# Optimization experiments

Measured on AMD Instinct MI355X. Metric: run time of the kernel, lower is better.

The kernel has to match this reference:

```python
import jax, jax.numpy as jnp
import numpy as np

B, N, E, H, D, F = 2, 4096, 128, 8, 16, 512
EPS = 1e-6


def _rms_norm(x, w):
    xf = x.astype(jnp.float32)
    n = xf * jax.lax.rsqrt(jnp.mean(xf * xf, axis=-1, keepdims=True) + EPS)
    return n.astype(x.dtype) * w


def setup_inputs() -> dict:
    key = jax.random.key(0)
    ks = jax.random.split(key, 12)
    s = 1.0 / np.sqrt(E)
    sf = 1.0 / np.sqrt(F)
    coords = jax.random.uniform(ks[10], (B, N, 2))
    dis = jnp.sqrt(jnp.sum((coords[:, :, None, :] - coords[:, None, :, :]) ** 2, -1))
    dis = dis * (1.0 - jnp.eye(N))  # zero diagonal
    return {
        "input1": jax.random.normal(ks[0], (B, N, E), jnp.float32),
        "dis_matrix": dis.astype(jnp.float32),
        "Wq": jax.random.uniform(ks[1], (E, E), jnp.float32, -s, s),
        "Wk": jax.random.uniform(ks[2], (E, E), jnp.float32, -s, s),
        "Wv": jax.random.uniform(ks[3], (E, E), jnp.float32, -s, s),
        "alpha": jnp.float32(1.0),
        "ln1_w": jnp.ones((E,), jnp.float32),
        "ln2_w": jnp.ones((E,), jnp.float32),
        "Wcomb": jax.random.uniform(ks[4], (E, E), jnp.float32, -s, s),
        "W1": jax.random.uniform(ks[5], (F, E), jnp.float32, -s, s),
        "b1": jax.random.uniform(ks[6], (F,), jnp.float32, -s, s),
        "W2": jax.random.uniform(ks[7], (E, F), jnp.float32, -sf, sf),
        "b2": jax.random.uniform(ks[8], (E,), jnp.float32, -sf, sf),
    }


def _sparse_attention_afm(x, dis_matrix, Wq, Wk, Wv, alpha):
    # project and split heads: [B,N,E] -> [B,H,N,D]
    def heads(w):
        return (x @ w.T).reshape(B, N, H, D).transpose(0, 2, 1, 3)
    q, k, v = heads(Wq), heads(Wk), heads(Wv)
    log2n = jnp.float32(np.log2(N))
    dis_weight = jnp.exp(-alpha * log2n * dis_matrix)  # [B,N,N] (i,j)
    k_weight = jnp.exp(k)  # [B,H,N,D]
    w1 = jnp.einsum('bij,bhik->bhjk', dis_weight, k_weight * v)
    w2 = jnp.einsum('bij,bhik->bhjk', dis_weight, k_weight)
    out = jax.nn.sigmoid(q) * (w1 / w2)  # [B,H,N,D]
    return out.transpose(0, 2, 1, 3).reshape(B, N, E)


def reference(input1, dis_matrix, Wq, Wk, Wv, alpha, ln1_w, ln2_w, Wcomb, W1, b1, W2, b2):
    h = _rms_norm(input1, ln1_w)
    attn = _sparse_attention_afm(h, dis_matrix, Wq, Wk, Wv, alpha)
    out1 = input1 + attn @ Wcomb.T
    h2 = _rms_norm(out1, ln2_w)
    ffn = jax.nn.relu(h2 @ W1.T + b1) @ W2.T + b2
    return out1 + ffn
```

## Files before the change

kernel.cpp:

```cpp
#include <hip/hip_runtime.h>

#define NTOK 4096
#define EDIM 128

typedef __attribute__((ext_vector_type(8))) short bf16x8;
typedef __attribute__((ext_vector_type(4))) float f32x4;

__device__ __forceinline__ ushort f2bf(float x) {
    union { float f; unsigned u; } c; c.f = x;
    unsigned r = c.u + 0x7FFF + ((c.u >> 16) & 1);
    return (ushort)(r >> 16);
}

__device__ __forceinline__ int swz64(int r, int k)  { return r * 64  + (k ^ ((r & 7) << 3)); }
__device__ __forceinline__ int swz128(int r, int k) { return r * 128 + (k ^ ((r & 7) << 3)); }

__device__ __forceinline__ void stage_w(const float* __restrict__ W, ushort* Bs) {
    const int t = threadIdx.x;
    const int br = t >> 1, h = (t & 1) * 64;
    const float* src = W + (size_t)br * 128 + h;
    ushort* dst = Bs + br * 136 + h;
#pragma unroll
    for (int j = 0; j < 8; ++j) {
        float4 u = *(const float4*)(src + j * 8);
        float4 v = *(const float4*)(src + j * 8 + 4);
        bf16x8 o;
        o[0] = (short)f2bf(u.x); o[1] = (short)f2bf(u.y);
        o[2] = (short)f2bf(u.z); o[3] = (short)f2bf(u.w);
        o[4] = (short)f2bf(v.x); o[5] = (short)f2bf(v.y);
        o[6] = (short)f2bf(v.z); o[7] = (short)f2bf(v.w);
        *(bf16x8*)(dst + j * 8) = o;
    }
}

__device__ __forceinline__ void gemm128(const ushort* __restrict__ As,
                                        const ushort* __restrict__ Bs,
                                        f32x4 (&acc)[2][2], int lane, int wv) {
    const int m15 = lane & 15, kq = (lane >> 4) * 8, c0w = wv * 32;
#pragma unroll
    for (int kc = 0; kc < 4; ++kc) {
        int ko = kc * 32 + kq;
        bf16x8 a0 = *(const bf16x8*)&As[m15 * 136 + ko];
        bf16x8 a1 = *(const bf16x8*)&As[(16 + m15) * 136 + ko];
        bf16x8 b0 = *(const bf16x8*)&Bs[(c0w + m15) * 136 + ko];
        bf16x8 b1 = *(const bf16x8*)&Bs[(c0w + 16 + m15) * 136 + ko];
        acc[0][0] = __builtin_amdgcn_mfma_f32_16x16x32_bf16(a0, b0, acc[0][0], 0, 0, 0);
        acc[0][1] = __builtin_amdgcn_mfma_f32_16x16x32_bf16(a0, b1, acc[0][1], 0, 0, 0);
        acc[1][0] = __builtin_amdgcn_mfma_f32_16x16x32_bf16(a1, b0, acc[1][0], 0, 0, 0);
        acc[1][1] = __builtin_amdgcn_mfma_f32_16x16x32_bf16(a1, b1, acc[1][1], 0, 0, 0);
    }
}

__device__ __forceinline__ void gemm_dirB(const ushort* __restrict__ As,
                                          const ushort* __restrict__ W, int ldb,
                                          f32x4 (&acc)[2][2], int lane, int wv) {
    const int m15 = lane & 15, kq = (lane >> 4) * 8, c0w = wv * 32;
#pragma unroll
    for (int kc = 0; kc < 4; ++kc) {
        int ko = kc * 32 + kq;
        bf16x8 a0 = *(const bf16x8*)&As[swz128(m15, ko)];
        bf16x8 a1 = *(const bf16x8*)&As[swz128(16 + m15, ko)];
        bf16x8 b0 = *(const bf16x8*)&W[(size_t)(c0w + m15) * ldb + ko];
        bf16x8 b1 = *(const bf16x8*)&W[(size_t)(c0w + 16 + m15) * ldb + ko];
        acc[0][0] = __builtin_amdgcn_mfma_f32_16x16x32_bf16(a0, b0, acc[0][0], 0, 0, 0);
        acc[0][1] = __builtin_amdgcn_mfma_f32_16x16x32_bf16(a0, b1, acc[0][1], 0, 0, 0);
        acc[1][0] = __builtin_amdgcn_mfma_f32_16x16x32_bf16(a1, b0, acc[1][0], 0, 0, 0);
        acc[1][1] = __builtin_amdgcn_mfma_f32_16x16x32_bf16(a1, b1, acc[1][1], 0, 0, 0);
    }
}

__launch_bounds__(256, 2)
__global__ void qkv_k(const float* __restrict__ input1, const float* __restrict__ ln1w,
                      const float* __restrict__ Wq, const float* __restrict__ Wk,
                      const float* __restrict__ Wv,
                      const float* __restrict__ Wc, const float* __restrict__ W1,
                      const float* __restrict__ W2, ushort* __restrict__ Wbf,
                      float* __restrict__ sigq, ushort* __restrict__ Mt) {
    const int bx = blockIdx.x;
    if (bx >= 256) {
        int g = ((bx - 256) * 256 + threadIdx.x) * 4;
        const float* src; ushort* dst;
        if (g < 16384)      { src = Wc + g;           dst = Wbf + 49152 + g; }
        else if (g < 81920) { src = W1 + (g - 16384); dst = Wbf + 65536 + (g - 16384); }
        else                { src = W2 + (g - 81920); dst = Wbf + 131072 + (g - 81920); }
        float4 u = *(const float4*)src;
        ushort4 o; o.x = f2bf(u.x); o.y = f2bf(u.y); o.z = f2bf(u.z); o.w = f2bf(u.w);
        *(ushort4*)dst = o;
        return;
    }
    __shared__ ushort As[32 * 136];
    __shared__ ushort Bs0[128 * 136];
    __shared__ ushort Bs1[128 * 136];
    const int t = threadIdx.x, lane = t & 63, wv = t >> 6;
    const int m15 = lane & 15, quad = lane >> 4, c0w = wv * 32;
    const int M0 = bx * 32;

    {
        const int row = t >> 3, seg = t & 7;
        const float* xp = input1 + (size_t)(M0 + row) * 128 + seg * 16;
        float4 x[4]; float ss = 0.f;
#pragma unroll
        for (int i = 0; i < 4; ++i) {
            x[i] = *(const float4*)(xp + i * 4);
            ss += x[i].x * x[i].x + x[i].y * x[i].y + x[i].z * x[i].z + x[i].w * x[i].w;
        }
        ss += __shfl_down(ss, 4, 8);
        ss += __shfl_down(ss, 2, 8);
        ss += __shfl_down(ss, 1, 8);
        ss = __shfl(ss, 0, 8);
        float rr = rsqrtf(ss * (1.0f / 128.0f) + 1e-6f);
#pragma unroll
        for (int i = 0; i < 4; ++i) {
            float4 w4 = *(const float4*)&ln1w[seg * 16 + i * 4];
            ushort4 o;
            o.x = f2bf(x[i].x * rr * w4.x);
            o.y = f2bf(x[i].y * rr * w4.y);
            o.z = f2bf(x[i].z * rr * w4.z);
            o.w = f2bf(x[i].w * rr * w4.w);
            *(ushort4*)&As[row * 136 + seg * 16 + i * 4] = o;
        }
    }
    stage_w(Wq, Bs0);
    __syncthreads();
    {
        f32x4 acc[2][2] = {};
        gemm128(As, Bs0, acc, lane, wv);
        stage_w(Wk, Bs1);
#pragma unroll
        for (int mi = 0; mi < 2; ++mi)
#pragma unroll
            for (int ni = 0; ni < 2; ++ni)
#pragma unroll
                for (int r = 0; r < 4; ++r) {
                    int row = M0 + mi * 16 + quad * 4 + r;
                    int lc  = c0w + ni * 16 + m15;
                    sigq[(size_t)row * 128 + lc] = 1.0f / (1.0f + __expf(-acc[mi][ni][r]));
                }
    }
    __syncthreads();
    f32x4 acck[2][2] = {};
    gemm128(As, Bs1, acck, lane, wv);
    stage_w(Wv, Bs0);
    __syncthreads();
    f32x4 accv[2][2] = {};
    gemm128(As, Bs0, accv, lane, wv);
    const int b = M0 >> 12, i0 = M0 & (NTOK - 1);
#pragma unroll
    for (int mi = 0; mi < 2; ++mi)
#pragma unroll
        for (int ni = 0; ni < 2; ++ni) {
            int e = c0w + ni * 16 + m15;
            ushort* mt0 = Mt + ((size_t)b * 256 + e) * NTOK;
            ushort* mt1 = mt0 + (size_t)128 * NTOK;
            int ib = i0 + mi * 16 + quad * 4;
            ushort4 pv, pk;
            float kw0 = __expf(acck[mi][ni][0]); pv.x = f2bf(kw0 * accv[mi][ni][0]); pk.x = f2bf(kw0);
            float kw1 = __expf(acck[mi][ni][1]); pv.y = f2bf(kw1 * accv[mi][ni][1]); pk.y = f2bf(kw1);
            float kw2 = __expf(acck[mi][ni][2]); pv.z = f2bf(kw2 * accv[mi][ni][2]); pk.z = f2bf(kw2);
            float kw3 = __expf(acck[mi][ni][3]); pv.w = f2bf(kw3 * accv[mi][ni][3]); pk.w = f2bf(kw3);
            *(ushort4*)&mt0[ib] = pv;
            *(ushort4*)&mt1[ib] = pk;
        }
}

__launch_bounds__(512, 2)
__global__ void big_gemm_k(const float* __restrict__ dis, const float* __restrict__ alphap,
                           const ushort* __restrict__ Mt,
                           float* __restrict__ P0, float* __restrict__ P1) {
    __shared__ ushort As[2][64 * 64];
    const int t = threadIdx.x, lane = t & 63, wv = t >> 6;
    const int m15 = lane & 15, quad = lane >> 4, kq = quad * 8;
    const int b  = blockIdx.x & 1;
    const int s  = (blockIdx.x >> 1) & 1;
    const int j0 = (blockIdx.x >> 2) * 64;
    const float coefl2 = -alphap[0] * 12.0f * 1.44269504088896f;
    const float* disb = dis + (size_t)b * NTOK * NTOK;
    const ushort* Mtb = Mt + (size_t)b * 256 * NTOK;
    float* outp = ((s == 0) ? P0 : P1) + (size_t)b * NTOK * 256;
    const int k0 = s * (NTOK / 2);

    const int sr = t >> 3, sk = (t & 7) * 8;
    const float* arow = disb + (size_t)(j0 + sr) * NTOK + k0 + sk;
    const int c0 = wv * 32;
    const ushort* Bp = Mtb + (size_t)(c0 + m15) * NTOK + k0 + kq;
    const ushort* Bp1 = Bp + (size_t)16 * NTOK;

    f32x4 acc[4][2] = {};
    float4 fa0, fa1, fb0, fb1;
    bf16x8 pb[2][2], pbn[2][2];

    {
        float4 g0 = *(const float4*)(arow);
        float4 g1 = *(const float4*)(arow + 4);
        bf16x8 a8;
        a8[0] = (short)f2bf(exp2f(coefl2 * g0.x));
        a8[1] = (short)f2bf(exp2f(coefl2 * g0.y));
        a8[2] = (short)f2bf(exp2f(coefl2 * g0.z));
        a8[3] = (short)f2bf(exp2f(coefl2 * g0.w));
        a8[4] = (short)f2bf(exp2f(coefl2 * g1.x));
        a8[5] = (short)f2bf(exp2f(coefl2 * g1.y));
        a8[6] = (short)f2bf(exp2f(coefl2 * g1.z));
        a8[7] = (short)f2bf(exp2f(coefl2 * g1.w));
        *(bf16x8*)&As[0][swz64(sr, sk)] = a8;
        fa0 = *(const float4*)(arow + 64);
        fa1 = *(const float4*)(arow + 68);
#pragma unroll
        for (int kh = 0; kh < 2; ++kh) {
            pb[kh][0] = *(const bf16x8*)&Bp[kh * 32];
            pb[kh][1] = *(const bf16x8*)&Bp1[kh * 32];
        }
        __syncthreads();
    }

#define BIG_ITER(FAc0, FAc1, FAn0, FAn1, PBC, PBN, BUFC, BUFN, IT) do {         \
    {   int ia = (IT) + 2; int ka = (ia < 32) ? ia * 64 : 0;                    \
        FAn0 = *(const float4*)(arow + ka);                                     \
        FAn1 = *(const float4*)(arow + ka + 4);                                 \
        int ib = (IT) + 1; int kb_ = (ib < 32) ? ib * 64 : 0;                   \
        _Pragma("unroll") for (int kh = 0; kh < 2; ++kh) {                      \
            PBN[kh][0] = *(const bf16x8*)&Bp[kb_ + kh * 32];                    \
            PBN[kh][1] = *(const bf16x8*)&Bp1[kb_ + kh * 32];                   \
        } }                                                                     \
    __builtin_amdgcn_sched_barrier(0);                                          \
    {   bf16x8 a8;                                                              \
        a8[0] = (short)f2bf(exp2f(coefl2 * FAc0.x));                            \
        a8[1] = (short)f2bf(exp2f(coefl2 * FAc0.y));                            \
        a8[2] = (short)f2bf(exp2f(coefl2 * FAc0.z));                            \
        a8[3] = (short)f2bf(exp2f(coefl2 * FAc0.w));                            \
        a8[4] = (short)f2bf(exp2f(coefl2 * FAc1.x));                            \
        a8[5] = (short)f2bf(exp2f(coefl2 * FAc1.y));                            \
        a8[6] = (short)f2bf(exp2f(coefl2 * FAc1.z));                            \
        a8[7] = (short)f2bf(exp2f(coefl2 * FAc1.w));                            \
        *(bf16x8*)&BUFN[swz64(sr, sk)] = a8; }                                  \
    _Pragma("unroll") for (int kh = 0; kh < 2; ++kh) {                          \
        bf16x8 a0 = *(const bf16x8*)&BUFC[swz64(m15,      kh * 32 + kq)];       \
        bf16x8 a1 = *(const bf16x8*)&BUFC[swz64(16 + m15, kh * 32 + kq)];       \
        bf16x8 a2 = *(const bf16x8*)&BUFC[swz64(32 + m15, kh * 32 + kq)];       \
        bf16x8 a3 = *(const bf16x8*)&BUFC[swz64(48 + m15, kh * 32 + kq)];       \
        acc[0][0] = __builtin_amdgcn_mfma_f32_16x16x32_bf16(a0, PBC[kh][0], acc[0][0], 0, 0, 0); \
        acc[0][1] = __builtin_amdgcn_mfma_f32_16x16x32_bf16(a0, PBC[kh][1], acc[0][1], 0, 0, 0); \
        acc[1][0] = __builtin_amdgcn_mfma_f32_16x16x32_bf16(a1, PBC[kh][0], acc[1][0], 0, 0, 0); \
        acc[1][1] = __builtin_amdgcn_mfma_f32_16x16x32_bf16(a1, PBC[kh][1], acc[1][1], 0, 0, 0); \
        acc[2][0] = __builtin_amdgcn_mfma_f32_16x16x32_bf16(a2, PBC[kh][0], acc[2][0], 0, 0, 0); \
        acc[2][1] = __builtin_amdgcn_mfma_f32_16x16x32_bf16(a2, PBC[kh][1], acc[2][1], 0, 0, 0); \
        acc[3][0] = __builtin_amdgcn_mfma_f32_16x16x32_bf16(a3, PBC[kh][0], acc[3][0], 0, 0, 0); \
        acc[3][1] = __builtin_amdgcn_mfma_f32_16x16x32_bf16(a3, PBC[kh][1], acc[3][1], 0, 0, 0); \
    }                                                                           \
    __builtin_amdgcn_sched_barrier(0);                                          \
    asm volatile("s_waitcnt lgkmcnt(0)" ::: "memory");                          \
    __builtin_amdgcn_s_barrier();                                               \
    __builtin_amdgcn_sched_barrier(0);                                          \
} while (0)

#pragma unroll 1
    for (int u = 0; u < 16; ++u) {
        int IT = u * 2;
        BIG_ITER(fa0, fa1, fb0, fb1, pb, pbn, As[0], As[1], IT);
        BIG_ITER(fb0, fb1, fa0, fa1, pbn, pb, As[1], As[0], IT + 1);
    }
#undef BIG_ITER

#pragma unroll
    for (int mi = 0; mi < 4; ++mi)
#pragma unroll
        for (int ni = 0; ni < 2; ++ni)
#pragma unroll
            for (int r = 0; r < 4; ++r) {
                int j = j0 + mi * 16 + quad * 4 + r;
                int c = c0 + ni * 16 + m15;
                outp[(size_t)j * 256 + c] = acc[mi][ni][r];
            }
}

__launch_bounds__(256, 1)
__global__ void tail_k(const float* __restrict__ sigq,
                       const float* __restrict__ P0, const float* __restrict__ P1,
                       const ushort* __restrict__ Wbf,
                       const float* __restrict__ input1, const float* __restrict__ b1,
                       const float* __restrict__ b2, const float* __restrict__ ln2w,
                       float* __restrict__ out) {
    __shared__ ushort As[32 * 128];
    __shared__ ushort As2[32 * 128];
    __shared__ float  O[32][132];
    const int t = threadIdx.x, lane = t & 63, wv = t >> 6;
    const int m15 = lane & 15, quad = lane >> 4, c0w = wv * 32;
    const int M0 = blockIdx.x * 32;

    {
        const int ar = t >> 3, e0 = (t & 7) * 16;
        const int g = M0 + ar;
        const float4* sg  = (const float4*)(sigq + (size_t)g * 128 + e0);
        const float4* p0a = (const float4*)(P0 + (size_t)g * 256 + e0);
        const float4* p1a = (const float4*)(P1 + (size_t)g * 256 + e0);
        const float4* p0b = (const float4*)(P0 + (size_t)g * 256 + 128 + e0);
        const float4* p1b = (const float4*)(P1 + (size_t)g * 256 + 128 + e0);
#pragma unroll
        for (int i = 0; i < 4; ++i) {
            float4 s = sg[i];
            float4 u0 = p0a[i], u1 = p1a[i], d0 = p0b[i], d1 = p1b[i];
            ushort4 a;
            a.x = f2bf(s.x * (u0.x + u1.x) / (d0.x + d1.x));
            a.y = f2bf(s.y * (u0.y + u1.y) / (d0.y + d1.y));
            a.z = f2bf(s.z * (u0.z + u1.z) / (d0.z + d1.z));
            a.w = f2bf(s.w * (u0.w + u1.w) / (d0.w + d1.w));
            *(ushort4*)&As[swz128(ar, e0 + i * 4)] = a;
        }
    }
    __syncthreads();
    f32x4 acc[2][2] = {};
    gemm_dirB(As, Wbf + 49152, 128, acc, lane, wv);
#pragma unroll
    for (int mi = 0; mi < 2; ++mi)
#pragma unroll
        for (int ni = 0; ni < 2; ++ni)
#pragma unroll
            for (int r = 0; r < 4; ++r) {
                int rl  = mi * 16 + quad * 4 + r;
                int col = c0w + ni * 16 + m15;
                O[rl][col] = acc[mi][ni][r] + input1[(size_t)(M0 + rl) * 128 + col];
            }
    __syncthreads();
    {
        const int row = t >> 3, seg = t & 7;
        float4 x[4]; float ss = 0.f;
#pragma unroll
        for (int i = 0; i < 4; ++i) {
            x[i] = *(const float4*)&O[row][seg * 16 + i * 4];
            ss += x[i].x * x[i].x + x[i].y * x[i].y + x[i].z * x[i].z + x[i].w * x[i].w;
        }
        ss += __shfl_down(ss, 4, 8);
        ss += __shfl_down(ss, 2, 8);
        ss += __shfl_down(ss, 1, 8);
        ss = __shfl(ss, 0, 8);
        float rr = rsqrtf(ss * (1.0f / 128.0f) + 1e-6f);
#pragma unroll
        for (int i = 0; i < 4; ++i) {
            float4 w4 = *(const float4*)&ln2w[seg * 16 + i * 4];
            ushort4 o;
            o.x = f2bf(x[i].x * rr * w4.x);
            o.y = f2bf(x[i].y * rr * w4.y);
            o.z = f2bf(x[i].z * rr * w4.z);
            o.w = f2bf(x[i].w * rr * w4.w);
            *(ushort4*)&As[swz128(row, seg * 16 + i * 4)] = o;
        }
    }
    f32x4 aout[2][2] = {};
    for (int f0 = 0; f0 < 4; ++f0) {
        __syncthreads();
        f32x4 am[2][2] = {};
        gemm_dirB(As, Wbf + 65536 + f0 * 128 * 128, 128, am, lane, wv);
#pragma unroll
        for (int mi = 0; mi < 2; ++mi)
#pragma unroll
            for (int ni = 0; ni < 2; ++ni)
#pragma unroll
                for (int r = 0; r < 4; ++r) {
                    int rl  = mi * 16 + quad * 4 + r;
                    int col = c0w + ni * 16 + m15;
                    As2[swz128(rl, col)] = f2bf(fmaxf(am[mi][ni][r] + b1[f0 * 128 + col], 0.0f));
                }
        __syncthreads();
        gemm_dirB(As2, Wbf + 131072 + f0 * 128, 512, aout, lane, wv);
    }
#pragma unroll
    for (int mi = 0; mi < 2; ++mi)
#pragma unroll
        for (int ni = 0; ni < 2; ++ni)
#pragma unroll
            for (int r = 0; r < 4; ++r) {
                int rl  = mi * 16 + quad * 4 + r;
                int col = c0w + ni * 16 + m15;
                out[(size_t)(M0 + rl) * 128 + col] = (O[rl][col] + b2[col]) + aout[mi][ni][r];
            }
}

extern "C" void kernel_launch(void* const* d_in, const int* in_sizes, int n_in,
                              void* d_out, int out_size, void* d_ws, size_t ws_size,
                              hipStream_t stream) {
    const float* input1 = (const float*)d_in[0];
    const float* dis    = (const float*)d_in[1];
    const float* Wq     = (const float*)d_in[2];
    const float* Wk     = (const float*)d_in[3];
    const float* Wv     = (const float*)d_in[4];
    const float* alpha  = (const float*)d_in[5];
    const float* ln1    = (const float*)d_in[6];
    const float* ln2    = (const float*)d_in[7];
    const float* Wcomb  = (const float*)d_in[8];
    const float* W1     = (const float*)d_in[9];
    const float* b1     = (const float*)d_in[10];
    const float* W2     = (const float*)d_in[11];
    const float* b2     = (const float*)d_in[12];
    float* out = (float*)d_out;

    char* w8 = (char*)d_ws;
    ushort* Wbf  = (ushort*)(w8);
    float*  sigq = (float*)(w8 + (4u << 20));
    ushort* Mt   = (ushort*)(w8 + (8u << 20));
    float*  P0   = (float*)(w8 + (12u << 20));
    float*  P1   = (float*)(w8 + (20u << 20));

    qkv_k<<<dim3(400), 256, 0, stream>>>(input1, ln1, Wq, Wk, Wv,
                                         Wcomb, W1, W2, Wbf, sigq, Mt);
    big_gemm_k<<<dim3(256), 512, 0, stream>>>(dis, alpha, Mt, P0, P1);
    tail_k<<<dim3(256), 256, 0, stream>>>(sigq, P0, P1, Wbf, input1, b1, b2,
                                          ln2, out);
}
```

Measured before the change: 258.3 us.

## Split big GEMM K dimension four ways and halve tail tile rows

The main dis-weighted GEMM now splits its K reduction into four slices instead of two, launching 512 blocks that write four partial buffers. The tail kernel sums all four partials and processes 16 rows per block instead of 32, also launching 512 blocks. Both changes aim to fill more of the GPU's compute units. The cost is extra partial-sum traffic (two more 8MB buffers written and read), smaller MFMA tiles in the tail with less weight reuse, and higher occupancy hints that may constrain registers.

```diff
diff --git a/kernel.cpp b/kernel.cpp
--- a/kernel.cpp
+++ b/kernel.cpp
@@ -51,21 +51,18 @@
     }
 }
 
-__device__ __forceinline__ void gemm_dirB(const ushort* __restrict__ As,
-                                          const ushort* __restrict__ W, int ldb,
-                                          f32x4 (&acc)[2][2], int lane, int wv) {
+__device__ __forceinline__ void gemm16_dirB(const ushort* __restrict__ As,
+                                            const ushort* __restrict__ W, int ldb,
+                                            f32x4 (&acc)[2], int lane, int wv) {
     const int m15 = lane & 15, kq = (lane >> 4) * 8, c0w = wv * 32;
 #pragma unroll
     for (int kc = 0; kc < 4; ++kc) {
         int ko = kc * 32 + kq;
         bf16x8 a0 = *(const bf16x8*)&As[swz128(m15, ko)];
-        bf16x8 a1 = *(const bf16x8*)&As[swz128(16 + m15, ko)];
         bf16x8 b0 = *(const bf16x8*)&W[(size_t)(c0w + m15) * ldb + ko];
         bf16x8 b1 = *(const bf16x8*)&W[(size_t)(c0w + 16 + m15) * ldb + ko];
-        acc[0][0] = __builtin_amdgcn_mfma_f32_16x16x32_bf16(a0, b0, acc[0][0], 0, 0, 0);
-        acc[0][1] = __builtin_amdgcn_mfma_f32_16x16x32_bf16(a0, b1, acc[0][1], 0, 0, 0);
-        acc[1][0] = __builtin_amdgcn_mfma_f32_16x16x32_bf16(a1, b0, acc[1][0], 0, 0, 0);
-        acc[1][1] = __builtin_amdgcn_mfma_f32_16x16x32_bf16(a1, b1, acc[1][1], 0, 0, 0);
+        acc[0] = __builtin_amdgcn_mfma_f32_16x16x32_bf16(a0, b0, acc[0], 0, 0, 0);
+        acc[1] = __builtin_amdgcn_mfma_f32_16x16x32_bf16(a0, b1, acc[1], 0, 0, 0);
     }
 }
 
@@ -163,26 +160,27 @@
         }
 }
 
-__launch_bounds__(512, 2)
+__launch_bounds__(512, 4)
 __global__ void big_gemm_k(const float* __restrict__ dis, const float* __restrict__ alphap,
                            const ushort* __restrict__ Mt,
-                           float* __restrict__ P0, float* __restrict__ P1) {
+                           float* __restrict__ P0, float* __restrict__ P1,
+                           float* __restrict__ P2, float* __restrict__ P3) {
     __shared__ ushort As[2][64 * 64];
     const int t = threadIdx.x, lane = t & 63, wv = t >> 6;
     const int m15 = lane & 15, quad = lane >> 4, kq = quad * 8;
     const int b  = blockIdx.x & 1;
-    const int s  = (blockIdx.x >> 1) & 1;
-    const int j0 = (blockIdx.x >> 2) * 64;
+    const int s  = (blockIdx.x >> 1) & 3;
+    const int j0 = (blockIdx.x >> 3) * 64;
     const float coefl2 = -alphap[0] * 12.0f * 1.44269504088896f;
     const float* disb = dis + (size_t)b * NTOK * NTOK;
     const ushort* Mtb = Mt + (size_t)b * 256 * NTOK;
-    float* outp = ((s == 0) ? P0 : P1) + (size_t)b * NTOK * 256;
-    const int k0 = s * (NTOK / 2);
+    float* outp = (s == 0 ? P0 : s == 1 ? P1 : s == 2 ? P2 : P3) + (size_t)b * NTOK * 256;
+    const int k0 = s * (NTOK / 4);
 
     const int sr = t >> 3, sk = (t & 7) * 8;
     const float* arow = disb + (size_t)(j0 + sr) * NTOK + k0 + sk;
     const int c0 = wv * 32;
-    const ushort* Bp = Mtb + (size_t)(c0 + m15) * NTOK + k0 + kq;
+    const ushort* Bp  = Mtb + (size_t)(c0 + m15) * NTOK + k0 + kq;
     const ushort* Bp1 = Bp + (size_t)16 * NTOK;
 
     f32x4 acc[4][2] = {};
@@ -213,10 +211,10 @@
     }
 
 #define BIG_ITER(FAc0, FAc1, FAn0, FAn1, PBC, PBN, BUFC, BUFN, IT) do {         \
-    {   int ia = (IT) + 2; int ka = (ia < 32) ? ia * 64 : 0;                    \
+    {   int ia = (IT) + 2; int ka = (ia < 16) ? ia * 64 : 0;                    \
         FAn0 = *(const float4*)(arow + ka);                                     \
         FAn1 = *(const float4*)(arow + ka + 4);                                 \
-        int ib = (IT) + 1; int kb_ = (ib < 32) ? ib * 64 : 0;                   \
+        int ib = (IT) + 1; int kb_ = (ib < 16) ? ib * 64 : 0;                   \
         _Pragma("unroll") for (int kh = 0; kh < 2; ++kh) {                      \
             PBN[kh][0] = *(const bf16x8*)&Bp[kb_ + kh * 32];                    \
             PBN[kh][1] = *(const bf16x8*)&Bp1[kb_ + kh * 32];                   \
@@ -253,7 +251,7 @@
 } while (0)
 
 #pragma unroll 1
-    for (int u = 0; u < 16; ++u) {
+    for (int u = 0; u < 8; ++u) {
         int IT = u * 2;
         BIG_ITER(fa0, fa1, fb0, fb1, pb, pbn, As[0], As[1], IT);
         BIG_ITER(fb0, fb1, fa0, fa1, pbn, pb, As[1], As[0], IT + 1);
@@ -272,106 +270,109 @@
             }
 }
 
-__launch_bounds__(256, 1)
+__launch_bounds__(256, 2)
 __global__ void tail_k(const float* __restrict__ sigq,
                        const float* __restrict__ P0, const float* __restrict__ P1,
+                       const float* __restrict__ P2, const float* __restrict__ P3,
                        const ushort* __restrict__ Wbf,
                        const float* __restrict__ input1, const float* __restrict__ b1,
                        const float* __restrict__ b2, const float* __restrict__ ln2w,
                        float* __restrict__ out) {
-    __shared__ ushort As[32 * 128];
-    __shared__ ushort As2[32 * 128];
-    __shared__ float  O[32][132];
+    __shared__ ushort As[16 * 128];
+    __shared__ ushort As2[16 * 128];
+    __shared__ float  O[16][132];
     const int t = threadIdx.x, lane = t & 63, wv = t >> 6;
     const int m15 = lane & 15, quad = lane >> 4, c0w = wv * 32;
-    const int M0 = blockIdx.x * 32;
+    const int M0 = blockIdx.x * 16;
 
     {
-        const int ar = t >> 3, e0 = (t & 7) * 16;
+        const int ar = t >> 4, e0 = (t & 15) * 8;
         const int g = M0 + ar;
-        const float4* sg  = (const float4*)(sigq + (size_t)g * 128 + e0);
-        const float4* p0a = (const float4*)(P0 + (size_t)g * 256 + e0);
-        const float4* p1a = (const float4*)(P1 + (size_t)g * 256 + e0);
-        const float4* p0b = (const float4*)(P0 + (size_t)g * 256 + 128 + e0);
-        const float4* p1b = (const float4*)(P1 + (size_t)g * 256 + 128 + e0);
-#pragma unroll
-        for (int i = 0; i < 4; ++i) {
-            float4 s = sg[i];
-            float4 u0 = p0a[i], u1 = p1a[i], d0 = p0b[i], d1 = p1b[i];
+        const float* sg = sigq + (size_t)g * 128 + e0;
+        const float* pu0 = P0 + (size_t)g * 256 + e0;
+        const float* pu1 = P1 + (size_t)g * 256 + e0;
+        const float* pu2 = P2 + (size_t)g * 256 + e0;
+        const float* pu3 = P3 + (size_t)g * 256 + e0;
+#pragma unroll
+        for (int i = 0; i < 2; ++i) {
+            float4 s  = *(const float4*)(sg + i * 4);
+            float4 u0 = *(const float4*)(pu0 + i * 4);
+            float4 u1 = *(const float4*)(pu1 + i * 4);
+            float4 u2 = *(const float4*)(pu2 + i * 4);
+            float4 u3 = *(const float4*)(pu3 + i * 4);
+            float4 d0 = *(const float4*)(pu0 + 128 + i * 4);
+            float4 d1 = *(const float4*)(pu1 + 128 + i * 4);
+            float4 d2 = *(const float4*)(pu2 + 128 + i * 4);
+            float4 d3 = *(const float4*)(pu3 + 128 + i * 4);
             ushort4 a;
-            a.x = f2bf(s.x * (u0.x + u1.x) / (d0.x + d1.x));
-            a.y = f2bf(s.y * (u0.y + u1.y) / (d0.y + d1.y));
-            a.z = f2bf(s.z * (u0.z + u1.z) / (d0.z + d1.z));
-            a.w = f2bf(s.w * (u0.w + u1.w) / (d0.w + d1.w));
+            a.x = f2bf(s.x * ((u0.x + u1.x) + (u2.x + u3.x)) / ((d0.x + d1.x) + (d2.x + d3.x)));
+            a.y = f2bf(s.y * ((u0.y + u1.y) + (u2.y + u3.y)) / ((d0.y + d1.y) + (d2.y + d3.y)));
+            a.z = f2bf(s.z * ((u0.z + u1.z) + (u2.z + u3.z)) / ((d0.z + d1.z) + (d2.z + d3.z)));
+            a.w = f2bf(s.w * ((u0.w + u1.w) + (u2.w + u3.w)) / ((d0.w + d1.w) + (d2.w + d3.w)));
             *(ushort4*)&As[swz128(ar, e0 + i * 4)] = a;
         }
     }
     __syncthreads();
-    f32x4 acc[2][2] = {};
-    gemm_dirB(As, Wbf + 49152, 128, acc, lane, wv);
-#pragma unroll
-    for (int mi = 0; mi < 2; ++mi)
-#pragma unroll
-        for (int ni = 0; ni < 2; ++ni)
-#pragma unroll
-            for (int r = 0; r < 4; ++r) {
-                int rl  = mi * 16 + quad * 4 + r;
-                int col = c0w + ni * 16 + m15;
-                O[rl][col] = acc[mi][ni][r] + input1[(size_t)(M0 + rl) * 128 + col];
-            }
+    f32x4 acc[2] = {};
+    gemm16_dirB(As, Wbf + 49152, 128, acc, lane, wv);
+#pragma unroll
+    for (int ni = 0; ni < 2; ++ni)
+#pragma unroll
+        for (int r = 0; r < 4; ++r) {
+            int rl  = quad * 4 + r;
+            int col = c0w + ni * 16 + m15;
+            O[rl][col] = acc[ni][r] + input1[(size_t)(M0 + rl) * 128 + col];
+        }
     __syncthreads();
     {
-        const int row = t >> 3, seg = t & 7;
-        float4 x[4]; float ss = 0.f;
-#pragma unroll
-        for (int i = 0; i < 4; ++i) {
-            x[i] = *(const float4*)&O[row][seg * 16 + i * 4];
+        const int row = t >> 4, seg = t & 15;
+        float4 x[2]; float ss = 0.f;
+#pragma unroll
+        for (int i = 0; i < 2; ++i) {
+            x[i] = *(const float4*)&O[row][seg * 8 + i * 4];
             ss += x[i].x * x[i].x + x[i].y * x[i].y + x[i].z * x[i].z + x[i].w * x[i].w;
         }
-        ss += __shfl_down(ss, 4, 8);
-        ss += __shfl_down(ss, 2, 8);
-        ss += __shfl_down(ss, 1, 8);
-        ss = __shfl(ss, 0, 8);
+        ss += __shfl_down(ss, 8, 16);
+        ss += __shfl_down(ss, 4, 16);
+        ss += __shfl_down(ss, 2, 16);
+        ss += __shfl_down(ss, 1, 16);
+        ss = __shfl(ss, 0, 16);
         float rr = rsqrtf(ss * (1.0f / 128.0f) + 1e-6f);
 #pragma unroll
-        for (int i = 0; i < 4; ++i) {
-            float4 w4 = *(const float4*)&ln2w[seg * 16 + i * 4];
+        for (int i = 0; i < 2; ++i) {
+            float4 w4 = *(const float4*)&ln2w[seg * 8 + i * 4];
             ushort4 o;
             o.x = f2bf(x[i].x * rr * w4.x);
             o.y = f2bf(x[i].y * rr * w4.y);
             o.z = f2bf(x[i].z * rr * w4.z);
             o.w = f2bf(x[i].w * rr * w4.w);
-            *(ushort4*)&As[swz128(row, seg * 16 + i * 4)] = o;
-        }
-    }
-    f32x4 aout[2][2] = {};
+            *(ushort4*)&As[swz128(row, seg * 8 + i * 4)] = o;
+        }
+    }
+    f32x4 aout[2] = {};
     for (int f0 = 0; f0 < 4; ++f0) {
         __syncthreads();
-        f32x4 am[2][2] = {};
-        gemm_dirB(As, Wbf + 65536 + f0 * 128 * 128, 128, am, lane, wv);
-#pragma unroll
-        for (int mi = 0; mi < 2; ++mi)
-#pragma unroll
-            for (int ni = 0; ni < 2; ++ni)
-#pragma unroll
-                for (int r = 0; r < 4; ++r) {
-                    int rl  = mi * 16 + quad * 4 + r;
-                    int col = c0w + ni * 16 + m15;
-                    As2[swz128(rl, col)] = f2bf(fmaxf(am[mi][ni][r] + b1[f0 * 128 + col], 0.0f));
-                }
+        f32x4 am[2] = {};
+        gemm16_dirB(As, Wbf + 65536 + f0 * 128 * 128, 128, am, lane, wv);
+#pragma unroll
+        for (int ni = 0; ni < 2; ++ni)
+#pragma unroll
+            for (int r = 0; r < 4; ++r) {
+                int rl  = quad * 4 + r;
+                int col = c0w + ni * 16 + m15;
+                As2[swz128(rl, col)] = f2bf(fmaxf(am[ni][r] + b1[f0 * 128 + col], 0.0f));
+            }
         __syncthreads();
-        gemm_dirB(As2, Wbf + 131072 + f0 * 128, 512, aout, lane, wv);
-    }
-#pragma unroll
-    for (int mi = 0; mi < 2; ++mi)
-#pragma unroll
-        for (int ni = 0; ni < 2; ++ni)
-#pragma unroll
-            for (int r = 0; r < 4; ++r) {
-                int rl  = mi * 16 + quad * 4 + r;
-                int col = c0w + ni * 16 + m15;
-                out[(size_t)(M0 + rl) * 128 + col] = (O[rl][col] + b2[col]) + aout[mi][ni][r];
-            }
+        gemm16_dirB(As2, Wbf + 131072 + f0 * 128, 512, aout, lane, wv);
+    }
+#pragma unroll
+    for (int ni = 0; ni < 2; ++ni)
+#pragma unroll
+        for (int r = 0; r < 4; ++r) {
+            int rl  = quad * 4 + r;
+            int col = c0w + ni * 16 + m15;
+            out[(size_t)(M0 + rl) * 128 + col] = (O[rl][col] + b2[col]) + aout[ni][r];
+        }
 }
 
 extern "C" void kernel_launch(void* const* d_in, const int* in_sizes, int n_in,
@@ -398,10 +399,12 @@
     ushort* Mt   = (ushort*)(w8 + (8u << 20));
     float*  P0   = (float*)(w8 + (12u << 20));
     float*  P1   = (float*)(w8 + (20u << 20));
+    float*  P2   = (float*)(w8 + (28u << 20));
+    float*  P3   = (float*)(w8 + (36u << 20));
 
     qkv_k<<<dim3(400), 256, 0, stream>>>(input1, ln1, Wq, Wk, Wv,
                                          Wcomb, W1, W2, Wbf, sigq, Mt);
-    big_gemm_k<<<dim3(256), 512, 0, stream>>>(dis, alpha, Mt, P0, P1);
-    tail_k<<<dim3(256), 256, 0, stream>>>(sigq, P0, P1, Wbf, input1, b1, b2,
-                                          ln2, out);
-}
+    big_gemm_k<<<dim3(512), 512, 0, stream>>>(dis, alpha, Mt, P0, P1, P2, P3);
+    tail_k<<<dim3(512), 256, 0, stream>>>(sigq, P0, P1, P2, P3, Wbf, input1,
+                                          b1, b2, ln2, out);
+}
```

Result: slower. 268.3 us (+3.9%).

## Double big GEMM block to 1024 threads with 128-row tiles and 4-way split-K

Applied to the files above, without the earlier changes.

The distance-weighted GEMM now runs 1024-thread blocks. Each block covers 128 output rows split across two wave rows and a quarter of the K range, instead of 64 rows and half of K. The grid stays at 256 blocks, so each CU gets twice as many waves to hide the latency of the global loads and exp work. The cost is two extra partial-sum buffers: more workspace written, and more partials that the tail kernel must read and reduce. The aggressive launch bounds may also squeeze registers.

```diff
diff --git a/kernel.cpp b/kernel.cpp
--- a/kernel.cpp
+++ b/kernel.cpp
@@ -163,26 +163,29 @@
         }
 }
 
-__launch_bounds__(512, 2)
+__launch_bounds__(1024, 4)
 __global__ void big_gemm_k(const float* __restrict__ dis, const float* __restrict__ alphap,
                            const ushort* __restrict__ Mt,
-                           float* __restrict__ P0, float* __restrict__ P1) {
-    __shared__ ushort As[2][64 * 64];
+                           float* __restrict__ P0, float* __restrict__ P1,
+                           float* __restrict__ P2, float* __restrict__ P3) {
+    __shared__ ushort As[2][128 * 64];
     const int t = threadIdx.x, lane = t & 63, wv = t >> 6;
     const int m15 = lane & 15, quad = lane >> 4, kq = quad * 8;
+    const int wc = wv & 7, wr = wv >> 3;
     const int b  = blockIdx.x & 1;
-    const int s  = (blockIdx.x >> 1) & 1;
-    const int j0 = (blockIdx.x >> 2) * 64;
+    const int s  = (blockIdx.x >> 1) & 3;
+    const int j0 = (blockIdx.x >> 3) * 128;
     const float coefl2 = -alphap[0] * 12.0f * 1.44269504088896f;
     const float* disb = dis + (size_t)b * NTOK * NTOK;
     const ushort* Mtb = Mt + (size_t)b * 256 * NTOK;
-    float* outp = ((s == 0) ? P0 : P1) + (size_t)b * NTOK * 256;
-    const int k0 = s * (NTOK / 2);
+    float* outp = (s == 0 ? P0 : s == 1 ? P1 : s == 2 ? P2 : P3) + (size_t)b * NTOK * 256;
+    const int k0 = s * (NTOK / 4);
 
     const int sr = t >> 3, sk = (t & 7) * 8;
     const float* arow = disb + (size_t)(j0 + sr) * NTOK + k0 + sk;
-    const int c0 = wv * 32;
-    const ushort* Bp = Mtb + (size_t)(c0 + m15) * NTOK + k0 + kq;
+    const int c0 = wc * 32;
+    const int rb = wr * 64;
+    const ushort* Bp  = Mtb + (size_t)(c0 + m15) * NTOK + k0 + kq;
     const ushort* Bp1 = Bp + (size_t)16 * NTOK;
 
     f32x4 acc[4][2] = {};
@@ -213,10 +216,10 @@
     }
 
 #define BIG_ITER(FAc0, FAc1, FAn0, FAn1, PBC, PBN, BUFC, BUFN, IT) do {         \
-    {   int ia = (IT) + 2; int ka = (ia < 32) ? ia * 64 : 0;                    \
+    {   int ia = (IT) + 2; int ka = (ia < 16) ? ia * 64 : 0;                    \
         FAn0 = *(const float4*)(arow + ka);                                     \
         FAn1 = *(const float4*)(arow + ka + 4);                                 \
-        int ib = (IT) + 1; int kb_ = (ib < 32) ? ib * 64 : 0;                   \
+        int ib = (IT) + 1; int kb_ = (ib < 16) ? ib * 64 : 0;                   \
         _Pragma("unroll") for (int kh = 0; kh < 2; ++kh) {                      \
             PBN[kh][0] = *(const bf16x8*)&Bp[kb_ + kh * 32];                    \
             PBN[kh][1] = *(const bf16x8*)&Bp1[kb_ + kh * 32];                   \
@@ -233,10 +236,10 @@
         a8[7] = (short)f2bf(exp2f(coefl2 * FAc1.w));                            \
         *(bf16x8*)&BUFN[swz64(sr, sk)] = a8; }                                  \
     _Pragma("unroll") for (int kh = 0; kh < 2; ++kh) {                          \
-        bf16x8 a0 = *(const bf16x8*)&BUFC[swz64(m15,      kh * 32 + kq)];       \
-        bf16x8 a1 = *(const bf16x8*)&BUFC[swz64(16 + m15, kh * 32 + kq)];       \
-        bf16x8 a2 = *(const bf16x8*)&BUFC[swz64(32 + m15, kh * 32 + kq)];       \
-        bf16x8 a3 = *(const bf16x8*)&BUFC[swz64(48 + m15, kh * 32 + kq)];       \
+        bf16x8 a0 = *(const bf16x8*)&BUFC[swz64(rb + m15,      kh * 32 + kq)];  \
+        bf16x8 a1 = *(const bf16x8*)&BUFC[swz64(rb + 16 + m15, kh * 32 + kq)];  \
+        bf16x8 a2 = *(const bf16x8*)&BUFC[swz64(rb + 32 + m15, kh * 32 + kq)];  \
+        bf16x8 a3 = *(const bf16x8*)&BUFC[swz64(rb + 48 + m15, kh * 32 + kq)];  \
         acc[0][0] = __builtin_amdgcn_mfma_f32_16x16x32_bf16(a0, PBC[kh][0], acc[0][0], 0, 0, 0); \
         acc[0][1] = __builtin_amdgcn_mfma_f32_16x16x32_bf16(a0, PBC[kh][1], acc[0][1], 0, 0, 0); \
         acc[1][0] = __builtin_amdgcn_mfma_f32_16x16x32_bf16(a1, PBC[kh][0], acc[1][0], 0, 0, 0); \
@@ -253,7 +256,7 @@
 } while (0)
 
 #pragma unroll 1
-    for (int u = 0; u < 16; ++u) {
+    for (int u = 0; u < 8; ++u) {
         int IT = u * 2;
         BIG_ITER(fa0, fa1, fb0, fb1, pb, pbn, As[0], As[1], IT);
         BIG_ITER(fb0, fb1, fa0, fa1, pbn, pb, As[1], As[0], IT + 1);
@@ -266,7 +269,7 @@
         for (int ni = 0; ni < 2; ++ni)
 #pragma unroll
             for (int r = 0; r < 4; ++r) {
-                int j = j0 + mi * 16 + quad * 4 + r;
+                int j = j0 + rb + mi * 16 + quad * 4 + r;
                 int c = c0 + ni * 16 + m15;
                 outp[(size_t)j * 256 + c] = acc[mi][ni][r];
             }
@@ -275,6 +278,7 @@
 __launch_bounds__(256, 1)
 __global__ void tail_k(const float* __restrict__ sigq,
                        const float* __restrict__ P0, const float* __restrict__ P1,
+                       const float* __restrict__ P2, const float* __restrict__ P3,
                        const ushort* __restrict__ Wbf,
                        const float* __restrict__ input1, const float* __restrict__ b1,
                        const float* __restrict__ b2, const float* __restrict__ ln2w,
@@ -289,20 +293,27 @@
     {
         const int ar = t >> 3, e0 = (t & 7) * 16;
         const int g = M0 + ar;
-        const float4* sg  = (const float4*)(sigq + (size_t)g * 128 + e0);
-        const float4* p0a = (const float4*)(P0 + (size_t)g * 256 + e0);
-        const float4* p1a = (const float4*)(P1 + (size_t)g * 256 + e0);
-        const float4* p0b = (const float4*)(P0 + (size_t)g * 256 + 128 + e0);
-        const float4* p1b = (const float4*)(P1 + (size_t)g * 256 + 128 + e0);
+        const float* sg  = sigq + (size_t)g * 128 + e0;
+        const float* q0 = P0 + (size_t)g * 256 + e0;
+        const float* q1 = P1 + (size_t)g * 256 + e0;
+        const float* q2 = P2 + (size_t)g * 256 + e0;
+        const float* q3 = P3 + (size_t)g * 256 + e0;
 #pragma unroll
         for (int i = 0; i < 4; ++i) {
-            float4 s = sg[i];
-            float4 u0 = p0a[i], u1 = p1a[i], d0 = p0b[i], d1 = p1b[i];
+            float4 s  = *(const float4*)(sg + i * 4);
+            float4 u0 = *(const float4*)(q0 + i * 4);
+            float4 u1 = *(const float4*)(q1 + i * 4);
+            float4 u2 = *(const float4*)(q2 + i * 4);
+            float4 u3 = *(const float4*)(q3 + i * 4);
+            float4 d0 = *(const float4*)(q0 + 128 + i * 4);
+            float4 d1 = *(const float4*)(q1 + 128 + i * 4);
+            float4 d2 = *(const float4*)(q2 + 128 + i * 4);
+            float4 d3 = *(const float4*)(q3 + 128 + i * 4);
             ushort4 a;
-            a.x = f2bf(s.x * (u0.x + u1.x) / (d0.x + d1.x));
-            a.y = f2bf(s.y * (u0.y + u1.y) / (d0.y + d1.y));
-            a.z = f2bf(s.z * (u0.z + u1.z) / (d0.z + d1.z));
-            a.w = f2bf(s.w * (u0.w + u1.w) / (d0.w + d1.w));
+            a.x = f2bf(s.x * ((u0.x + u1.x) + (u2.x + u3.x)) / ((d0.x + d1.x) + (d2.x + d3.x)));
+            a.y = f2bf(s.y * ((u0.y + u1.y) + (u2.y + u3.y)) / ((d0.y + d1.y) + (d2.y + d3.y)));
+            a.z = f2bf(s.z * ((u0.z + u1.z) + (u2.z + u3.z)) / ((d0.z + d1.z) + (d2.z + d3.z)));
+            a.w = f2bf(s.w * ((u0.w + u1.w) + (u2.w + u3.w)) / ((d0.w + d1.w) + (d2.w + d3.w)));
             *(ushort4*)&As[swz128(ar, e0 + i * 4)] = a;
         }
     }
@@ -398,10 +409,12 @@
     ushort* Mt   = (ushort*)(w8 + (8u << 20));
     float*  P0   = (float*)(w8 + (12u << 20));
     float*  P1   = (float*)(w8 + (20u << 20));
+    float*  P2   = (float*)(w8 + (28u << 20));
+    float*  P3   = (float*)(w8 + (36u << 20));
 
     qkv_k<<<dim3(400), 256, 0, stream>>>(input1, ln1, Wq, Wk, Wv,
                                          Wcomb, W1, W2, Wbf, sigq, Mt);
-    big_gemm_k<<<dim3(256), 512, 0, stream>>>(dis, alpha, Mt, P0, P1);
-    tail_k<<<dim3(256), 256, 0, stream>>>(sigq, P0, P1, Wbf, input1, b1, b2,
-                                          ln2, out);
-}
+    big_gemm_k<<<dim3(256), 1024, 0, stream>>>(dis, alpha, Mt, P0, P1, P2, P3);
+    tail_k<<<dim3(256), 256, 0, stream>>>(sigq, P0, P1, P2, P3, Wbf, input1,
+                                          b1, b2, ln2, out);
+}
```

New measurement: 267.0 us. 1.03x slower.

## Widen big GEMM K-chunk to 256 with fewer barriers per block

Applied to the files above, without the earlier changes.

The distance-weight GEMM now stages 256-wide K chunks of exp(dis) in LDS instead of 64-wide chunks. Each thread prefetches eight float4 loads two chunks ahead, and the block syncs 8 times instead of 32. The B-operand (Mt) prefetch into registers is dropped; B fragments are now loaded from global memory inside the MFMA loop. This cuts barrier overhead, but LDS per block grows to 64 KB, which may limit occupancy under launch_bounds(512,2), and the B loads are now exposed.

```diff
diff --git a/kernel.cpp b/kernel.cpp
--- a/kernel.cpp
+++ b/kernel.cpp
@@ -12,8 +12,8 @@
     return (ushort)(r >> 16);
 }
 
-__device__ __forceinline__ int swz64(int r, int k)  { return r * 64  + (k ^ ((r & 7) << 3)); }
 __device__ __forceinline__ int swz128(int r, int k) { return r * 128 + (k ^ ((r & 7) << 3)); }
+__device__ __forceinline__ int swz256(int r, int k) { return r * 256 + (k ^ ((r & 7) << 3)); }
 
 __device__ __forceinline__ void stage_w(const float* __restrict__ W, ushort* Bs) {
     const int t = threadIdx.x;
@@ -167,7 +167,7 @@
 __global__ void big_gemm_k(const float* __restrict__ dis, const float* __restrict__ alphap,
                            const ushort* __restrict__ Mt,
                            float* __restrict__ P0, float* __restrict__ P1) {
-    __shared__ ushort As[2][64 * 64];
+    __shared__ ushort As[2][64 * 256];
     const int t = threadIdx.x, lane = t & 63, wv = t >> 6;
     const int m15 = lane & 15, quad = lane >> 4, kq = quad * 8;
     const int b  = blockIdx.x & 1;
@@ -179,86 +179,88 @@
     float* outp = ((s == 0) ? P0 : P1) + (size_t)b * NTOK * 256;
     const int k0 = s * (NTOK / 2);
 
-    const int sr = t >> 3, sk = (t & 7) * 8;
-    const float* arow = disb + (size_t)(j0 + sr) * NTOK + k0 + sk;
+    const int sr = t >> 3, sk8 = (t & 7) * 8;
+    const float* arow = disb + (size_t)(j0 + sr) * NTOK + k0 + sk8;
     const int c0 = wv * 32;
-    const ushort* Bp = Mtb + (size_t)(c0 + m15) * NTOK + k0 + kq;
+    const ushort* Bp  = Mtb + (size_t)(c0 + m15) * NTOK + k0 + kq;
     const ushort* Bp1 = Bp + (size_t)16 * NTOK;
 
+    float4 ra0, ra1, ra2, ra3, ra4, ra5, ra6, ra7;
+
+#define LOAD_CHUNK(BASE) do {                                                   \
+    ra0 = *(const float4*)(arow + (BASE));                                      \
+    ra1 = *(const float4*)(arow + (BASE) + 4);                                  \
+    ra2 = *(const float4*)(arow + (BASE) + 64);                                 \
+    ra3 = *(const float4*)(arow + (BASE) + 68);                                 \
+    ra4 = *(const float4*)(arow + (BASE) + 128);                                \
+    ra5 = *(const float4*)(arow + (BASE) + 132);                                \
+    ra6 = *(const float4*)(arow + (BASE) + 192);                                \
+    ra7 = *(const float4*)(arow + (BASE) + 196);                                \
+} while (0)
+
+#define EXP8(DST, RA, RB) do {                                                  \
+    DST[0] = (short)f2bf(exp2f(coefl2 * RA.x));                                 \
+    DST[1] = (short)f2bf(exp2f(coefl2 * RA.y));                                 \
+    DST[2] = (short)f2bf(exp2f(coefl2 * RA.z));                                 \
+    DST[3] = (short)f2bf(exp2f(coefl2 * RA.w));                                 \
+    DST[4] = (short)f2bf(exp2f(coefl2 * RB.x));                                 \
+    DST[5] = (short)f2bf(exp2f(coefl2 * RB.y));                                 \
+    DST[6] = (short)f2bf(exp2f(coefl2 * RB.z));                                 \
+    DST[7] = (short)f2bf(exp2f(coefl2 * RB.w));                                 \
+} while (0)
+
+#define EXPWRITE(BUF) do {                                                      \
+    bf16x8 w0, w1, w2, w3;                                                      \
+    EXP8(w0, ra0, ra1); EXP8(w1, ra2, ra3);                                     \
+    EXP8(w2, ra4, ra5); EXP8(w3, ra6, ra7);                                     \
+    *(bf16x8*)&BUF[swz256(sr, sk8)]       = w0;                                 \
+    *(bf16x8*)&BUF[swz256(sr, sk8 + 64)]  = w1;                                 \
+    *(bf16x8*)&BUF[swz256(sr, sk8 + 128)] = w2;                                 \
+    *(bf16x8*)&BUF[swz256(sr, sk8 + 192)] = w3;                                 \
+} while (0)
+
+    {
+        LOAD_CHUNK(0);
+        EXPWRITE(As[0]);
+        LOAD_CHUNK(256);
+        __syncthreads();
+    }
+
     f32x4 acc[4][2] = {};
-    float4 fa0, fa1, fb0, fb1;
-    bf16x8 pb[2][2], pbn[2][2];
-
-    {
-        float4 g0 = *(const float4*)(arow);
-        float4 g1 = *(const float4*)(arow + 4);
-        bf16x8 a8;
-        a8[0] = (short)f2bf(exp2f(coefl2 * g0.x));
-        a8[1] = (short)f2bf(exp2f(coefl2 * g0.y));
-        a8[2] = (short)f2bf(exp2f(coefl2 * g0.z));
-        a8[3] = (short)f2bf(exp2f(coefl2 * g0.w));
-        a8[4] = (short)f2bf(exp2f(coefl2 * g1.x));
-        a8[5] = (short)f2bf(exp2f(coefl2 * g1.y));
-        a8[6] = (short)f2bf(exp2f(coefl2 * g1.z));
-        a8[7] = (short)f2bf(exp2f(coefl2 * g1.w));
-        *(bf16x8*)&As[0][swz64(sr, sk)] = a8;
-        fa0 = *(const float4*)(arow + 64);
-        fa1 = *(const float4*)(arow + 68);
-#pragma unroll
-        for (int kh = 0; kh < 2; ++kh) {
-            pb[kh][0] = *(const bf16x8*)&Bp[kh * 32];
-            pb[kh][1] = *(const bf16x8*)&Bp1[kh * 32];
-        }
-        __syncthreads();
-    }
-
-#define BIG_ITER(FAc0, FAc1, FAn0, FAn1, PBC, PBN, BUFC, BUFN, IT) do {         \
-    {   int ia = (IT) + 2; int ka = (ia < 32) ? ia * 64 : 0;                    \
-        FAn0 = *(const float4*)(arow + ka);                                     \
-        FAn1 = *(const float4*)(arow + ka + 4);                                 \
-        int ib = (IT) + 1; int kb_ = (ib < 32) ? ib * 64 : 0;                   \
-        _Pragma("unroll") for (int kh = 0; kh < 2; ++kh) {                      \
-            PBN[kh][0] = *(const bf16x8*)&Bp[kb_ + kh * 32];                    \
-            PBN[kh][1] = *(const bf16x8*)&Bp1[kb_ + kh * 32];                   \
-        } }                                                                     \
-    __builtin_amdgcn_sched_barrier(0);                                          \
-    {   bf16x8 a8;                                                              \
-        a8[0] = (short)f2bf(exp2f(coefl2 * FAc0.x));                            \
-        a8[1] = (short)f2bf(exp2f(coefl2 * FAc0.y));                            \
-        a8[2] = (short)f2bf(exp2f(coefl2 * FAc0.z));                            \
-        a8[3] = (short)f2bf(exp2f(coefl2 * FAc0.w));                            \
-        a8[4] = (short)f2bf(exp2f(coefl2 * FAc1.x));                            \
-        a8[5] = (short)f2bf(exp2f(coefl2 * FAc1.y));                            \
-        a8[6] = (short)f2bf(exp2f(coefl2 * FAc1.z));                            \
-        a8[7] = (short)f2bf(exp2f(coefl2 * FAc1.w));                            \
-        *(bf16x8*)&BUFN[swz64(sr, sk)] = a8; }                                  \
-    _Pragma("unroll") for (int kh = 0; kh < 2; ++kh) {                          \
-        bf16x8 a0 = *(const bf16x8*)&BUFC[swz64(m15,      kh * 32 + kq)];       \
-        bf16x8 a1 = *(const bf16x8*)&BUFC[swz64(16 + m15, kh * 32 + kq)];       \
-        bf16x8 a2 = *(const bf16x8*)&BUFC[swz64(32 + m15, kh * 32 + kq)];       \
-        bf16x8 a3 = *(const bf16x8*)&BUFC[swz64(48 + m15, kh * 32 + kq)];       \
-        acc[0][0] = __builtin_amdgcn_mfma_f32_16x16x32_bf16(a0, PBC[kh][0], acc[0][0], 0, 0, 0); \
-        acc[0][1] = __builtin_amdgcn_mfma_f32_16x16x32_bf16(a0, PBC[kh][1], acc[0][1], 0, 0, 0); \
-        acc[1][0] = __builtin_amdgcn_mfma_f32_16x16x32_bf16(a1, PBC[kh][0], acc[1][0], 0, 0, 0); \
-        acc[1][1] = __builtin_amdgcn_mfma_f32_16x16x32_bf16(a1, PBC[kh][1], acc[1][1], 0, 0, 0); \
-        acc[2][0] = __builtin_amdgcn_mfma_f32_16x16x32_bf16(a2, PBC[kh][0], acc[2][0], 0, 0, 0); \
-        acc[2][1] = __builtin_amdgcn_mfma_f32_16x16x32_bf16(a2, PBC[kh][1], acc[2][1], 0, 0, 0); \
-        acc[3][0] = __builtin_amdgcn_mfma_f32_16x16x32_bf16(a3, PBC[kh][0], acc[3][0], 0, 0, 0); \
-        acc[3][1] = __builtin_amdgcn_mfma_f32_16x16x32_bf16(a3, PBC[kh][1], acc[3][1], 0, 0, 0); \
-    }                                                                           \
-    __builtin_amdgcn_sched_barrier(0);                                          \
-    asm volatile("s_waitcnt lgkmcnt(0)" ::: "memory");                          \
-    __builtin_amdgcn_s_barrier();                                               \
-    __builtin_amdgcn_sched_barrier(0);                                          \
-} while (0)
-
-#pragma unroll 1
-    for (int u = 0; u < 16; ++u) {
-        int IT = u * 2;
-        BIG_ITER(fa0, fa1, fb0, fb1, pb, pbn, As[0], As[1], IT);
-        BIG_ITER(fb0, fb1, fa0, fa1, pbn, pb, As[1], As[0], IT + 1);
-    }
-#undef BIG_ITER
+#pragma unroll 2
+    for (int c = 0; c < 8; ++c) {
+        ushort* bufC = As[c & 1];
+        ushort* bufN = As[(c + 1) & 1];
+        if (c < 7) EXPWRITE(bufN);
+        if (c < 6) LOAD_CHUNK((c + 2) * 256);
+        const int cb = c * 256;
+#pragma unroll
+        for (int si = 0; si < 4; ++si) {
+#pragma unroll
+            for (int kh = 0; kh < 2; ++kh) {
+                int col = si * 64 + kh * 32 + kq;
+                bf16x8 a0 = *(const bf16x8*)&bufC[swz256(m15,      col)];
+                bf16x8 a1 = *(const bf16x8*)&bufC[swz256(16 + m15, col)];
+                bf16x8 a2 = *(const bf16x8*)&bufC[swz256(32 + m15, col)];
+                bf16x8 a3 = *(const bf16x8*)&bufC[swz256(48 + m15, col)];
+                bf16x8 bk0 = *(const bf16x8*)&Bp[cb + si * 64 + kh * 32];
+                bf16x8 bk1 = *(const bf16x8*)&Bp1[cb + si * 64 + kh * 32];
+                acc[0][0] = __builtin_amdgcn_mfma_f32_16x16x32_bf16(a0, bk0, acc[0][0], 0, 0, 0);
+                acc[0][1] = __builtin_amdgcn_mfma_f32_16x16x32_bf16(a0, bk1, acc[0][1], 0, 0, 0);
+                acc[1][0] = __builtin_amdgcn_mfma_f32_16x16x32_bf16(a1, bk0, acc[1][0], 0, 0, 0);
+                acc[1][1] = __builtin_amdgcn_mfma_f32_16x16x32_bf16(a1, bk1, acc[1][1], 0, 0, 0);
+                acc[2][0] = __builtin_amdgcn_mfma_f32_16x16x32_bf16(a2, bk0, acc[2][0], 0, 0, 0);
+                acc[2][1] = __builtin_amdgcn_mfma_f32_16x16x32_bf16(a2, bk1, acc[2][1], 0, 0, 0);
+                acc[3][0] = __builtin_amdgcn_mfma_f32_16x16x32_bf16(a3, bk0, acc[3][0], 0, 0, 0);
+                acc[3][1] = __builtin_amdgcn_mfma_f32_16x16x32_bf16(a3, bk1, acc[3][1], 0, 0, 0);
+            }
+        }
+        asm volatile("s_waitcnt lgkmcnt(0)" ::: "memory");
+        __builtin_amdgcn_s_barrier();
+    }
+#undef LOAD_CHUNK
+#undef EXP8
+#undef EXPWRITE
 
 #pragma unroll
     for (int mi = 0; mi < 4; ++mi)
```

New measurement: 271.5 us. 1.05x slower.
